# Kernel optimization log

Hardware: AMD Instinct MI355X
Metric: run time of the kernel (lower is better)

The kernel has to match this reference:

```python
import jax, jax.numpy as jnp
import numpy as np

CAPACITY = 8_388_608  # 2**23, power of two -> leftmost_leaf == capacity
N_UPDATES = 1_048_576  # 2**20


def setup_inputs() -> dict:
    key = jax.random.key(0)
    k1, k2, k3 = jax.random.split(key, 3)
    # Existing tree buffer; values[1] is root, values[CAPACITY:2*CAPACITY] are leaves.
    tree_values = jax.random.uniform(k1, (2 * CAPACITY,), dtype=jnp.float32)
    # Distinct leaf indices in [0, CAPACITY): torch scatter-assign with duplicate
    # indices is nondeterministic, so the meaningful case is distinct indices.
    indices = jax.random.permutation(k2, CAPACITY)[:N_UPDATES].astype(jnp.int32)
    values = jax.random.uniform(k3, (N_UPDATES,), dtype=jnp.float32)
    return {"tree_values": tree_values, "indices": indices, "values": values}


def reference(tree_values, indices, values):
    """SegmentTree.__setitem__ with op=add: set leaves, propagate sums to root.

    Returns the updated (2*capacity,) tree buffer.
    """
    capacity = tree_values.shape[0] // 2  # static python int
    depth = int(capacity).bit_length() - 1  # log2(capacity) levels to the root
    # _index_to_leaf: with power-of-two capacity, leaf = idx + capacity (no wrap).
    leaf = indices.astype(jnp.int32) + capacity
    tree = tree_values.at[leaf].set(values)
    idx = leaf
    # Original does torch.unique(idx//2) per level purely as an optimization;
    # duplicate parents recompute the identical value, so plain scatter-set of
    # op(left_child, right_child) is the same math and jit-friendly.
    for _ in range(depth):
        idx = idx // 2
        parent = tree[2 * idx] + tree[2 * idx + 1]
        tree = tree.at[idx].set(parent)
    return tree
```

## Files before the change

### kernel.cpp

```cpp
#include <hip/hip_runtime.h>


typedef unsigned int uint;
typedef unsigned char uchar;
typedef unsigned long long ull;

#define NBINS 1024
#define BCAP  2048

__device__ __forceinline__ ull pc64(ull c) {
    ull x = (c | (c >> 1)) & 0x5555555555555555ull;
    x = (x | (x >> 1))  & 0x3333333333333333ull;
    x = (x | (x >> 2))  & 0x0F0F0F0F0F0F0F0Full;
    x = (x | (x >> 4))  & 0x00FF00FF00FF00FFull;
    x = (x | (x >> 8))  & 0x0000FFFF0000FFFFull;
    x = (x | (x >> 16)) & 0x00000000FFFFFFFFull;
    return x;
}

__global__ __launch_bounds__(1024)
void bin_kernel(const int* __restrict__ idx,
                const float* __restrict__ val,
                uint* __restrict__ cnt,
                uint2* __restrict__ bins) {
    __shared__ uint hist[NBINS];
    __shared__ uint rbase[NBINS];
    const int tid = threadIdx.x;
    hist[tid] = 0u;
    __syncthreads();

    const int g = blockIdx.x * 1024 + tid;
    int4   j4 = ((const int4*)idx)[g];
    float4 v4 = ((const float4*)val)[g];
    uint  j[4] = { (uint)j4.x, (uint)j4.y, (uint)j4.z, (uint)j4.w };
    float v[4] = { v4.x, v4.y, v4.z, v4.w };

    #pragma unroll
    for (int e = 0; e < 4; ++e) atomicAdd(&hist[j[e] >> 13], 1u);
    __syncthreads();

    uint h = hist[tid];
    rbase[tid] = h ? atomicAdd(&cnt[tid], h) : 0u;
    hist[tid] = 0u;
    __syncthreads();

    #pragma unroll
    for (int e = 0; e < 4; ++e) {
        uint bin = j[e] >> 13;
        uint r = rbase[bin] + atomicAdd(&hist[bin], 1u);
        if (r < BCAP)
            bins[((size_t)bin << 11) + r] =
                make_uint2(j[e] & 8191u, __float_as_uint(v[e]));
    }
}

__global__ __launch_bounds__(1024)
void merge_kernel(const float* __restrict__ tree,
                  const uint* __restrict__ cnt,
                  const uint2* __restrict__ bins,
                  uchar* __restrict__ l13flag,
                  float* __restrict__ out, int C) {
    __shared__ float slv[8192];
    __shared__ uchar sfl[8192];
    __shared__ float s9v[16];
    __shared__ uint  s9d[16];

    const int b    = blockIdx.x;
    const int tid  = threadIdx.x;
    const int wv   = tid >> 6;
    const int lane = tid & 63;

    ((uint2*)sfl)[tid] = make_uint2(0u, 0u);
    __syncthreads();
    uint c = cnt[b];
    if (c > BCAP) c = BCAP;
    const uint2* mybin = bins + ((size_t)b << 11);
    for (uint k = tid; k < c; k += 1024u) {
        uint2 e = mybin[k];
        slv[e.x] = __uint_as_float(e.y);
        sfl[e.x] = 1;
    }
    __syncthreads();

    const int leaf0  = tid * 8;
    const int gleaf0 = b * 8192 + leaf0;

    uint2 fw = *(const uint2*)&sfl[leaf0];
    float4 la = *(const float4*)&slv[leaf0];
    float4 lb = *(const float4*)&slv[leaf0 + 4];
    float4 ta = *(const float4*)(tree + C + gleaf0);
    float4 tb = *(const float4*)(tree + C + gleaf0 + 4);

    float l0 = (fw.x & 0x000000FFu) ? la.x : ta.x;
    float l1 = (fw.x & 0x0000FF00u) ? la.y : ta.y;
    float l2 = (fw.x & 0x00FF0000u) ? la.z : ta.z;
    float l3 = (fw.x & 0xFF000000u) ? la.w : ta.w;
    float l4 = (fw.y & 0x000000FFu) ? lb.x : tb.x;
    float l5 = (fw.y & 0x0000FF00u) ? lb.y : tb.y;
    float l6 = (fw.y & 0x00FF0000u) ? lb.z : tb.z;
    float l7 = (fw.y & 0xFF000000u) ? lb.w : tb.w;

    *(float4*)(out + C + gleaf0)     = make_float4(l0, l1, l2, l3);
    *(float4*)(out + C + gleaf0 + 4) = make_float4(l4, l5, l6, l7);

    uint d10 = (fw.x & 0x0000FFFFu) != 0u;
    uint d11 = (fw.x & 0xFFFF0000u) != 0u;
    uint d12 = (fw.y & 0x0000FFFFu) != 0u;
    uint d13 = (fw.y & 0xFFFF0000u) != 0u;
    float4 t1 = *(const float4*)(tree + (C >> 1) + (gleaf0 >> 1));
    float4 v1;
    v1.x = d10 ? l0 + l1 : t1.x;
    v1.y = d11 ? l2 + l3 : t1.y;
    v1.z = d12 ? l4 + l5 : t1.z;
    v1.w = d13 ? l6 + l7 : t1.w;
    *(float4*)(out + (C >> 1) + (gleaf0 >> 1)) = v1;

    float2 t2 = *(const float2*)(tree + (C >> 2) + (gleaf0 >> 2));
    uint d20 = d10 | d11, d21 = d12 | d13;
    float2 v2;
    v2.x = d20 ? v1.x + v1.y : t2.x;
    v2.y = d21 ? v1.z + v1.w : t2.y;
    *(float2*)(out + (C >> 2) + (gleaf0 >> 2)) = v2;

    float t3v = tree[(C >> 3) + (gleaf0 >> 3)];
    uint d3 = d20 | d21;
    float v = d3 ? v2.x + v2.y : t3v;
    out[(C >> 3) + (gleaf0 >> 3)] = v;

    const int r = b * 16 + wv;
    ull m = __ballot(d3 != 0u);
    #pragma unroll
    for (int lvl = 4; lvl <= 9; ++lvl) {
        float a  = __shfl(v, 2 * lane, 64);
        float bb = __shfl(v, 2 * lane + 1, 64);
        m = pc64(m);
        int n = 64 >> (lvl - 3);
        if (lane < n) {
            int node = (C >> lvl) + (r << (9 - lvl)) + lane;
            uint dd = (uint)(m >> lane) & 1u;
            v = dd ? a + bb : tree[node];
            out[node] = v;
        }
    }
    if (lane == 0) { s9v[wv] = v; s9d[wv] = (uint)(m & 1ull); }
    __syncthreads();

    if (wv == 0) {
        float vv = lane < 16 ? s9v[lane] : 0.f;
        uint dd  = lane < 16 ? s9d[lane] : 0u;
        ull mm = __ballot(dd != 0u);
        #pragma unroll
        for (int lvl = 10; lvl <= 13; ++lvl) {
            float a  = __shfl(vv, 2 * lane, 64);
            float bb = __shfl(vv, 2 * lane + 1, 64);
            mm = pc64(mm);
            int n = 1 << (13 - lvl);
            if (lane < n) {
                int node = (C >> lvl) + (b << (13 - lvl)) + lane;
                uint d2 = (uint)(mm >> lane) & 1u;
                vv = d2 ? a + bb : tree[node];
                out[node] = vv;
            }
        }
        if (lane == 0) l13flag[b] = (uchar)(mm & 1ull);
    }
}

__global__ __launch_bounds__(1024)
void tail_kernel(const float* __restrict__ tree,
                 const uchar* __restrict__ l13flag,
                 float* __restrict__ out) {
    __shared__ float s16v[16];
    __shared__ uint  s16d[16];
    const int t = threadIdx.x, w = t >> 6, lane = t & 63;

    float v = out[1024 + t];
    uint d = l13flag[t];

    ull m = __ballot(d != 0u);
    #pragma unroll
    for (int M = 512; M >= 16; M >>= 1) {
        float a  = __shfl(v, 2 * lane, 64);
        float bb = __shfl(v, 2 * lane + 1, 64);
        m = pc64(m);
        int nw = M >> 4;
        if (lane < nw) {
            int node = M + nw * w + lane;
            uint dd = (uint)(m >> lane) & 1u;
            v = dd ? a + bb : tree[node];
            out[node] = v;
        }
    }
    if (lane == 0) { s16v[w] = v; s16d[w] = (uint)(m & 1ull); }
    __syncthreads();

    if (w == 0) {
        float vv = lane < 16 ? s16v[lane] : 0.f;
        uint dd  = lane < 16 ? s16d[lane] : 0u;
        ull mm = __ballot(dd != 0u);
        #pragma unroll
        for (int M = 8; M >= 1; M >>= 1) {
            float a  = __shfl(vv, 2 * lane, 64);
            float bb = __shfl(vv, 2 * lane + 1, 64);
            mm = pc64(mm);
            if (lane < M) {
                uint d2 = (uint)(mm >> lane) & 1u;
                vv = d2 ? a + bb : tree[M + lane];
                out[M + lane] = vv;
            }
        }
        if (lane == 0) out[0] = tree[0];
    }
}

extern "C" void kernel_launch(void* const* d_in, const int* in_sizes, int n_in,
                              void* d_out, int out_size, void* d_ws, size_t ws_size,
                              hipStream_t stream) {
    const float* tree    = (const float*)d_in[0];
    const int*   indices = (const int*)d_in[1];
    const float* values  = (const float*)d_in[2];
    float* out = (float*)d_out;

    const int two_cap = in_sizes[0];
    const int C       = two_cap >> 1;
    const int nupd    = in_sizes[1];

    uchar* ws = (uchar*)d_ws;
    uint*  cnt  = (uint*)ws;
    uchar* l13  = ws + 4096;
    uint2* bins = (uint2*)(ws + 32768);

    hipMemsetAsync(cnt, 0, NBINS * sizeof(uint), stream);
    bin_kernel<<<nupd / 4096, 1024, 0, stream>>>(indices, values, cnt, bins);
    merge_kernel<<<C / 8192, 1024, 0, stream>>>(tree, cnt, bins, l13, out, C);
    tail_kernel<<<1, 1024, 0, stream>>>(tree, l13, out);
}
```

Measured before the change: 146.0 us.

## Use per-block bin chunks without global atomics and fold tail into merge

Each bin block now writes its updates into a private 32-slot chunk per destination bin, recording per-block counts. This replaces the global atomic reservation and the count memset. The merge kernel gathers from the 256 chunks using all threads in parallel. A last-block-done ticket runs the top-level reduction inside the merge kernel, which removes the separate tail launch. Chunks are capped at KCAP=32 per block per bin, so updates beyond that cap would be dropped silently.

```diff
diff --git a/kernel.cpp b/kernel.cpp
--- a/kernel.cpp
+++ b/kernel.cpp
@@ -6,7 +6,8 @@
 typedef unsigned long long ull;
 
 #define NBINS 1024
-#define BCAP  2048
+#define NBB   256
+#define KCAP  32
 
 __device__ __forceinline__ ull pc64(ull c) {
     ull x = (c | (c >> 1)) & 0x5555555555555555ull;
@@ -21,49 +22,51 @@
 __global__ __launch_bounds__(1024)
 void bin_kernel(const int* __restrict__ idx,
                 const float* __restrict__ val,
-                uint* __restrict__ cnt,
-                uint2* __restrict__ bins) {
-    __shared__ uint hist[NBINS];
-    __shared__ uint rbase[NBINS];
+                uchar* __restrict__ cnts,
+                uint2* __restrict__ bins,
+                uint* __restrict__ done) {
+    __shared__ uint cur[NBINS];
     const int tid = threadIdx.x;
-    hist[tid] = 0u;
-    __syncthreads();
-
-    const int g = blockIdx.x * 1024 + tid;
+    const int b   = blockIdx.x;
+    cur[tid] = 0u;
+    __syncthreads();
+
+    const int g = b * 1024 + tid;
     int4   j4 = ((const int4*)idx)[g];
     float4 v4 = ((const float4*)val)[g];
     uint  j[4] = { (uint)j4.x, (uint)j4.y, (uint)j4.z, (uint)j4.w };
     float v[4] = { v4.x, v4.y, v4.z, v4.w };
 
     #pragma unroll
-    for (int e = 0; e < 4; ++e) atomicAdd(&hist[j[e] >> 13], 1u);
-    __syncthreads();
-
-    uint h = hist[tid];
-    rbase[tid] = h ? atomicAdd(&cnt[tid], h) : 0u;
-    hist[tid] = 0u;
-    __syncthreads();
-
-    #pragma unroll
     for (int e = 0; e < 4; ++e) {
-        uint bin = j[e] >> 13;
-        uint r = rbase[bin] + atomicAdd(&hist[bin], 1u);
-        if (r < BCAP)
-            bins[((size_t)bin << 11) + r] =
+        uint bin  = j[e] >> 13;
+        uint slot = atomicAdd(&cur[bin], 1u);
+        if (slot < KCAP)
+            bins[(((size_t)bin * NBB + b) << 5) + slot] =
                 make_uint2(j[e] & 8191u, __float_as_uint(v[e]));
     }
+    __syncthreads();
+
+    uint c = cur[tid];
+    cnts[b * NBINS + tid] = (uchar)(c > KCAP ? KCAP : c);
+    if (b == 0 && tid == 0) *done = 0u;
 }
 
 __global__ __launch_bounds__(1024)
 void merge_kernel(const float* __restrict__ tree,
-                  const uint* __restrict__ cnt,
+                  const uchar* __restrict__ cnts,
                   const uint2* __restrict__ bins,
                   uchar* __restrict__ l13flag,
+                  uint* __restrict__ done,
                   float* __restrict__ out, int C) {
     __shared__ float slv[8192];
     __shared__ uchar sfl[8192];
+    __shared__ uchar scnt[NBB];
     __shared__ float s9v[16];
     __shared__ uint  s9d[16];
+    __shared__ uint  sticket;
+    __shared__ float s16v[16];
+    __shared__ uint  s16d[16];
 
     const int b    = blockIdx.x;
     const int tid  = threadIdx.x;
@@ -71,14 +74,20 @@
     const int lane = tid & 63;
 
     ((uint2*)sfl)[tid] = make_uint2(0u, 0u);
-    __syncthreads();
-    uint c = cnt[b];
-    if (c > BCAP) c = BCAP;
-    const uint2* mybin = bins + ((size_t)b << 11);
-    for (uint k = tid; k < c; k += 1024u) {
-        uint2 e = mybin[k];
-        slv[e.x] = __uint_as_float(e.y);
-        sfl[e.x] = 1;
+    if (tid < NBB) scnt[tid] = cnts[tid * NBINS + b];
+    __syncthreads();
+
+    {
+        const int c  = tid & 255;
+        const int g8 = (tid >> 8) * 8;
+        int n = (int)scnt[c];
+        int hi = n < g8 + 8 ? n : g8 + 8;
+        const uint2* chunk = bins + (((size_t)b * NBB + c) << 5);
+        for (int s = g8; s < hi; ++s) {
+            uint2 e = chunk[s];
+            slv[e.x] = __uint_as_float(e.y);
+            sfl[e.x] = 1;
+        }
     }
     __syncthreads();
 
@@ -164,52 +173,57 @@
         }
         if (lane == 0) l13flag[b] = (uchar)(mm & 1ull);
     }
-}
-
-__global__ __launch_bounds__(1024)
-void tail_kernel(const float* __restrict__ tree,
-                 const uchar* __restrict__ l13flag,
-                 float* __restrict__ out) {
-    __shared__ float s16v[16];
-    __shared__ uint  s16d[16];
-    const int t = threadIdx.x, w = t >> 6, lane = t & 63;
-
-    float v = out[1024 + t];
-    uint d = l13flag[t];
-
-    ull m = __ballot(d != 0u);
-    #pragma unroll
-    for (int M = 512; M >= 16; M >>= 1) {
-        float a  = __shfl(v, 2 * lane, 64);
-        float bb = __shfl(v, 2 * lane + 1, 64);
-        m = pc64(m);
-        int nw = M >> 4;
-        if (lane < nw) {
-            int node = M + nw * w + lane;
-            uint dd = (uint)(m >> lane) & 1u;
-            v = dd ? a + bb : tree[node];
-            out[node] = v;
-        }
-    }
-    if (lane == 0) { s16v[w] = v; s16d[w] = (uint)(m & 1ull); }
-    __syncthreads();
-
-    if (w == 0) {
-        float vv = lane < 16 ? s16v[lane] : 0.f;
-        uint dd  = lane < 16 ? s16d[lane] : 0u;
-        ull mm = __ballot(dd != 0u);
+    __syncthreads();
+
+    if (tid == 0) {
+        __threadfence();
+        sticket = atomicAdd(done, 1u);
+    }
+    __syncthreads();
+    if (sticket != (uint)gridDim.x - 1u) return;
+
+    if (tid == 0) __threadfence();
+    __syncthreads();
+
+    {
+        const int t = tid, w = tid >> 6;
+        float tv = out[(C >> 13) + t];
+        uint td  = l13flag[t];
+
+        ull m2 = __ballot(td != 0u);
         #pragma unroll
-        for (int M = 8; M >= 1; M >>= 1) {
-            float a  = __shfl(vv, 2 * lane, 64);
-            float bb = __shfl(vv, 2 * lane + 1, 64);
-            mm = pc64(mm);
-            if (lane < M) {
-                uint d2 = (uint)(mm >> lane) & 1u;
-                vv = d2 ? a + bb : tree[M + lane];
-                out[M + lane] = vv;
+        for (int M = 512; M >= 16; M >>= 1) {
+            float a  = __shfl(tv, 2 * lane, 64);
+            float bb = __shfl(tv, 2 * lane + 1, 64);
+            m2 = pc64(m2);
+            int nw = M >> 4;
+            if (lane < nw) {
+                int node = M + nw * w + lane;
+                uint dd = (uint)(m2 >> lane) & 1u;
+                tv = dd ? a + bb : tree[node];
+                out[node] = tv;
             }
         }
-        if (lane == 0) out[0] = tree[0];
+        if (lane == 0) { s16v[w] = tv; s16d[w] = (uint)(m2 & 1ull); }
+        __syncthreads();
+
+        if (w == 0) {
+            float vv = lane < 16 ? s16v[lane] : 0.f;
+            uint dd  = lane < 16 ? s16d[lane] : 0u;
+            ull mm = __ballot(dd != 0u);
+            #pragma unroll
+            for (int M = 8; M >= 1; M >>= 1) {
+                float a  = __shfl(vv, 2 * lane, 64);
+                float bb = __shfl(vv, 2 * lane + 1, 64);
+                mm = pc64(mm);
+                if (lane < M) {
+                    uint d2 = (uint)(mm >> lane) & 1u;
+                    vv = d2 ? a + bb : tree[M + lane];
+                    out[M + lane] = vv;
+                }
+            }
+            if (lane == 0) out[0] = tree[0];
+        }
     }
 }
 
@@ -226,12 +240,13 @@
     const int nupd    = in_sizes[1];
 
     uchar* ws = (uchar*)d_ws;
-    uint*  cnt  = (uint*)ws;
-    uchar* l13  = ws + 4096;
-    uint2* bins = (uint2*)(ws + 32768);
-
-    hipMemsetAsync(cnt, 0, NBINS * sizeof(uint), stream);
-    bin_kernel<<<nupd / 4096, 1024, 0, stream>>>(indices, values, cnt, bins);
-    merge_kernel<<<C / 8192, 1024, 0, stream>>>(tree, cnt, bins, l13, out, C);
-    tail_kernel<<<1, 1024, 0, stream>>>(tree, l13, out);
-}
+    uint*  done = (uint*)ws;
+    uchar* l13  = ws + 1024;
+    uchar* cnts = ws + 4096;
+    uint2* bins = (uint2*)(ws + 524288);
+
+    bin_kernel<<<nupd / 4096, 1024, 0, stream>>>(indices, values, cnts,
+                                                 bins, done);
+    merge_kernel<<<C / 8192, 1024, 0, stream>>>(tree, cnts, bins, l13,
+                                                done, out, C);
+}
```

Result: slower. 190.1 us (+30.2%).
